# Performance work log

Measured on AMD Instinct MI355X. Metric: run time of the kernel, lower is better.

Reference implementation:

```python
import jax, jax.numpy as jnp
import numpy as np

D_MODEL = 1024
H = 16
D_K = D_MODEL // H
B = 4
S = 2048
NEG = -1.0e9


def setup_inputs() -> dict:
    key = jax.random.key(0)
    ks = jax.random.split(key, 12)
    scale = 1.0 / np.sqrt(D_MODEL)
    inp = {
        "q": jax.random.normal(ks[0], (B, S, D_MODEL), jnp.float32),
        "k": jax.random.normal(ks[1], (B, S, D_MODEL), jnp.float32),
        "v": jax.random.normal(ks[2], (B, S, D_MODEL), jnp.float32),
        "mask": jax.random.randint(ks[3], (1, 1, S, S), 0, 2, jnp.int32),
        # nn.Linear params: y = x @ W.T + b
        "Wq": jax.random.normal(ks[4], (D_MODEL, D_MODEL), jnp.float32) * scale,
        "bq": jnp.zeros((D_MODEL,), jnp.float32),
        "Wk": jax.random.normal(ks[5], (D_MODEL, D_MODEL), jnp.float32) * scale,
        "bk": jnp.zeros((D_MODEL,), jnp.float32),
        "Wv": jax.random.normal(ks[6], (D_MODEL, D_MODEL), jnp.float32) * scale,
        "bv": jnp.zeros((D_MODEL,), jnp.float32),
        "Wo": jax.random.normal(ks[7], (D_MODEL, D_MODEL), jnp.float32) * scale,
        "bo": jnp.zeros((D_MODEL,), jnp.float32),
    }
    return inp


def reference(q, k, v, mask, Wq, bq, Wk, bk, Wv, bv, Wo, bo):
    # QKV projections (torch Linear: x @ W.T + b)
    query = q @ Wq.T + bq                       # [B,S,D]
    key_ = k @ Wk.T + bk
    value = v @ Wv.T + bv
    # [B,S,D] -> [B,H,S,d_k]
    def split_heads(x):
        return x.reshape(B, S, H, D_K).transpose(0, 2, 1, 3)
    query, key_, value = split_heads(query), split_heads(key_), split_heads(value)
    # scaled dot-product attention
    scores = jnp.einsum("bhqd,bhkd->bhqk", query, key_) / np.sqrt(D_K)
    scores = jnp.where(mask == 0, NEG, scores)  # masked_fill(mask==0, -1e9)
    attn = jax.nn.softmax(scores, axis=-1)      # dropout p=0 -> identity
    x = jnp.einsum("bhqk,bhkd->bhqd", attn, value)
    # merge heads and output projection
    x = x.transpose(0, 2, 1, 3).reshape(B, S, D_MODEL)
    return x @ Wo.T + bo
```

## Files before the change

kernel.cpp:

```cpp
#include <hip/hip_runtime.h>
#include <hip/hip_bf16.h>

typedef __bf16 bf16;
typedef __bf16 bf16x8 __attribute__((ext_vector_type(8)));
typedef __bf16 bf16x4 __attribute__((ext_vector_type(4)));
typedef float  f32x4v __attribute__((ext_vector_type(4)));

#define MFMA16(a, b, c) __builtin_amdgcn_mfma_f32_16x16x32_bf16((a), (b), (c), 0, 0, 0)

static constexpr int D_MODEL = 1024;
static constexpr int NH      = 16;
static constexpr int DK      = 64;
static constexpr int BATCH   = 4;
static constexpr int SEQ     = 2048;

__device__ __forceinline__ void glds16(const void* g, void* l) {
    __builtin_amdgcn_global_load_lds((const __attribute__((address_space(1))) void*)g,
                                     (__attribute__((address_space(3))) void*)l, 16, 0, 0);
}

struct CvtArgs {
    const float* s[7];
    bf16* d[7];
    int n[7];
};

__global__ __launch_bounds__(256) void cvt7(CvtArgs a) {
    const int which = blockIdx.y;
    const int i = (blockIdx.x * 256 + threadIdx.x) * 8;
    if (i >= a.n[which]) return;
    const float4 v0 = *(const float4*)(a.s[which] + i);
    const float4 v1 = *(const float4*)(a.s[which] + i + 4);
    bf16x8 o = {(bf16)v0.x, (bf16)v0.y, (bf16)v0.z, (bf16)v0.w,
                (bf16)v1.x, (bf16)v1.y, (bf16)v1.z, (bf16)v1.w};
    *(bf16x8*)(a.d[which] + i) = o;
}

__global__ __launch_bounds__(256) void mask_prep(const int* __restrict__ m,
                                                 bf16* __restrict__ Mr) {
    const int o = blockIdx.x * 256 + threadIdx.x;
    const int row = o >> 11, j = o & 2047;
    const int g = j >> 6, idx = j & 63;
    const int incol = (g << 6) + ((idx & 3) << 4) + (idx >> 2);
    Mr[o] = m[row * 2048 + incol] ? (bf16)0.0f : (bf16)-16384.0f;
}

template <int MODE>
__global__ __launch_bounds__(256) void gemm_bt(const bf16* __restrict__ A,
                                               const bf16* __restrict__ W,
                                               const float* __restrict__ bias,
                                               void* __restrict__ outv) {
    __shared__ bf16 Als[128 * 32];
    __shared__ bf16 Bls[128 * 32];

    const int tid  = threadIdx.x;
    const int wave = tid >> 6;
    const int lane = tid & 63;
    const int l15  = lane & 15;
    const int quad = lane >> 4;
    const int m0   = blockIdx.y * 128;
    const int n0   = blockIdx.x * 128;
    const int wm   = (wave >> 1) * 64;
    const int wn   = (wave & 1) * 64;

    f32x4v acc[4][4];
#pragma unroll
    for (int i = 0; i < 4; ++i)
#pragma unroll
        for (int j = 0; j < 4; ++j) acc[i][j] = (f32x4v){0.f, 0.f, 0.f, 0.f};

    const int r_a    = wave * 16 + (lane >> 2);
    const int c_a    = (lane & 3) * 8;
    const int ldsoff = wave * 512;

    for (int k0 = 0; k0 < 1024; k0 += 32) {
        __syncthreads();
#pragma unroll
        for (int p = 0; p < 2; ++p) {
            const int row = p * 64 + r_a;
            glds16(A + (size_t)(m0 + row) * 1024 + k0 + c_a, &Als[p * 2048 + ldsoff]);
            glds16(W + (size_t)(n0 + row) * 1024 + k0 + c_a, &Bls[p * 2048 + ldsoff]);
        }
        __syncthreads();

        bf16x8 af[4], bfr[4];
#pragma unroll
        for (int i = 0; i < 4; ++i)
            af[i] = *(const bf16x8*)(&Als[(wm + i * 16 + l15) * 32 + quad * 8]);
#pragma unroll
        for (int j = 0; j < 4; ++j)
            bfr[j] = *(const bf16x8*)(&Bls[(wn + j * 16 + l15) * 32 + quad * 8]);
#pragma unroll
        for (int i = 0; i < 4; ++i)
#pragma unroll
            for (int j = 0; j < 4; ++j) acc[i][j] = MFMA16(af[i], bfr[j], acc[i][j]);
    }

#pragma unroll
    for (int j = 0; j < 4; ++j) {
        const int col = n0 + wn + j * 16 + l15;
        const float bs = bias[col];
        const int h = col >> 6, dk = col & 63;
        if (MODE == 1) {
            bf16* out = (bf16*)outv;
            const int sg = m0 + wm;
            const int bb = sg >> 11, sb = sg & 2047;
            const size_t rowbase = ((size_t)((bb * NH + h) * 64 + dk)) * SEQ + sb;
#pragma unroll
            for (int reg = 0; reg < 4; ++reg) {
                bf16x4 v = {(bf16)(acc[0][j][reg] + bs), (bf16)(acc[1][j][reg] + bs),
                            (bf16)(acc[2][j][reg] + bs), (bf16)(acc[3][j][reg] + bs)};
                *(bf16x4*)(&out[rowbase + (quad * 4 + reg) * 4]) = v;
            }
        } else {
#pragma unroll
            for (int i = 0; i < 4; ++i) {
                const int r4 = m0 + wm + i * 16 + quad * 4;
                const int b = r4 >> 11, sb = r4 & 2047;
                if (MODE == 2) {
                    float* out = (float*)outv;
#pragma unroll
                    for (int reg = 0; reg < 4; ++reg)
                        out[(size_t)(r4 + reg) * 1024 + col] = acc[i][j][reg] + bs;
                } else {
                    bf16* out = (bf16*)outv;
#pragma unroll
                    for (int reg = 0; reg < 4; ++reg)
                        out[((size_t)(b * NH + h) * SEQ + sb + reg) * 64 + dk] =
                            (bf16)(acc[i][j][reg] + bs);
                }
            }
        }
    }
}

__global__ __launch_bounds__(256, 4) void attn_kernel(const bf16* __restrict__ Qh,
                                                      const bf16* __restrict__ Kh,
                                                      const bf16* __restrict__ Vtg,
                                                      const bf16* __restrict__ Mr,
                                                      bf16* __restrict__ Xout) {
    __shared__ bf16 Kls[4096];
    __shared__ bf16 Vls[4096];
    __shared__ bf16 Pls[256 * 72];

    const int tid  = threadIdx.x;
    const int wave = tid >> 6;
    const int lane = tid & 63;
    const int l15  = lane & 15;
    const int quad = lane >> 4;
    const int bh   = blockIdx.x;
    const int q0   = blockIdx.y * 256;

    const size_t base = (size_t)bh * SEQ * DK;
    const bf16* Q  = Qh + base;
    const bf16* K  = Kh + base;
    const bf16* Vg = Vtg + base;

    const int qw = q0 + wave * 64;
    bf16x8 aq[4][2];
#pragma unroll
    for (int rb = 0; rb < 4; ++rb)
#pragma unroll
        for (int hf = 0; hf < 2; ++hf)
            aq[rb][hf] = *(const bf16x8*)(Q + (size_t)(qw + rb * 16 + l15) * 64 +
                                          hf * 32 + quad * 8);

    bf16x8 ones;
#pragma unroll
    for (int t = 0; t < 8; ++t) ones[t] = (bf16)1.0f;

    f32x4v acc[4][4];
    f32x4v sacc[4];
#pragma unroll
    for (int rb = 0; rb < 4; ++rb) {
        sacc[rb] = (f32x4v){0.f, 0.f, 0.f, 0.f};
#pragma unroll
        for (int x = 0; x < 4; ++x) acc[rb][x] = (f32x4v){0.f, 0.f, 0.f, 0.f};
    }

    constexpr float CLOG = 0.125f * 1.4426950408889634f;
    const bf16* mbase = Mr + (size_t)(qw + quad * 4) * 2048 + l15 * 4;

    for (int kt = 0; kt < SEQ; kt += 64) {
        __syncthreads();
#pragma unroll
        for (int p = 0; p < 2; ++p) {
            const int kc = wave * 2 + p;
            glds16(K + (size_t)(kt + lane) * 64 + kc * 8, &Kls[kc * 512]);
            glds16(Vg + (size_t)lane * SEQ + kt + kc * 8, &Vls[kc * 512]);
        }
        bf16x4 mv[4][4];
#pragma unroll
        for (int rb = 0; rb < 4; ++rb)
#pragma unroll
            for (int reg = 0; reg < 4; ++reg)
                mv[rb][reg] =
                    *(const bf16x4*)(mbase + (size_t)(rb * 16 + reg) * 2048 + kt);
        __syncthreads();

        bf16x8 bk[4][2];
#pragma unroll
        for (int n16 = 0; n16 < 4; ++n16)
#pragma unroll
            for (int kk = 0; kk < 2; ++kk)
                bk[n16][kk] = *(const bf16x8*)(&Kls[((kk * 4 + quad) * 64 + n16 * 16 + l15) * 8]);

#pragma unroll
        for (int rb = 0; rb < 4; ++rb) {
            f32x4v sv[4];
            __builtin_amdgcn_s_setprio(1);
#pragma unroll
            for (int n16 = 0; n16 < 4; ++n16) {
                f32x4v t = (f32x4v){0.f, 0.f, 0.f, 0.f};
                t = MFMA16(aq[rb][0], bk[n16][0], t);
                t = MFMA16(aq[rb][1], bk[n16][1], t);
                sv[n16] = t;
            }
            __builtin_amdgcn_s_setprio(0);
            const int prow0 = wave * 64 + rb * 16 + quad * 4;
#pragma unroll
            for (int reg = 0; reg < 4; ++reg) {
                const float e0 = exp2f(fmaf(sv[0][reg], CLOG, (float)mv[rb][reg][0]));
                const float e1 = exp2f(fmaf(sv[1][reg], CLOG, (float)mv[rb][reg][1]));
                const float e2 = exp2f(fmaf(sv[2][reg], CLOG, (float)mv[rb][reg][2]));
                const float e3 = exp2f(fmaf(sv[3][reg], CLOG, (float)mv[rb][reg][3]));
                bf16x4 p4 = {(bf16)e0, (bf16)e1, (bf16)e2, (bf16)e3};
                *(bf16x4*)(&Pls[(prow0 + reg) * 72 + l15 * 4]) = p4;
            }
        }

        bf16x8 pf[4][2];
#pragma unroll
        for (int rb = 0; rb < 4; ++rb)
#pragma unroll
            for (int kc2 = 0; kc2 < 2; ++kc2)
                pf[rb][kc2] = *(const bf16x8*)(&Pls[(wave * 64 + rb * 16 + l15) * 72 +
                                                    kc2 * 32 + quad * 8]);

        __builtin_amdgcn_s_setprio(1);
#pragma unroll
        for (int rb = 0; rb < 4; ++rb) {
            sacc[rb] = MFMA16(pf[rb][0], ones, sacc[rb]);
            sacc[rb] = MFMA16(pf[rb][1], ones, sacc[rb]);
        }
#pragma unroll
        for (int nt = 0; nt < 4; ++nt) {
            const bf16x8 bv0 = *(const bf16x8*)(&Vls[(quad * 64 + nt * 16 + l15) * 8]);
            const bf16x8 bv1 = *(const bf16x8*)(&Vls[((4 + quad) * 64 + nt * 16 + l15) * 8]);
#pragma unroll
            for (int rb = 0; rb < 4; ++rb) {
                acc[rb][nt] = MFMA16(pf[rb][0], bv0, acc[rb][nt]);
                acc[rb][nt] = MFMA16(pf[rb][1], bv1, acc[rb][nt]);
            }
        }
        __builtin_amdgcn_s_setprio(0);
    }

    const int b = bh >> 4, h = bh & 15;
#pragma unroll
    for (int rb = 0; rb < 4; ++rb) {
        float rinv[4];
#pragma unroll
        for (int reg = 0; reg < 4; ++reg) rinv[reg] = 1.0f / sacc[rb][reg];
#pragma unroll
        for (int nt = 0; nt < 4; ++nt)
#pragma unroll
            for (int reg = 0; reg < 4; ++reg) {
                const int sg = qw + rb * 16 + quad * 4 + reg;
                Xout[(size_t)(b * SEQ + sg) * D_MODEL + h * 64 + nt * 16 + l15] =
                    (bf16)(acc[rb][nt][reg] * rinv[reg]);
            }
    }
}

extern "C" void kernel_launch(void* const* d_in, const int* in_sizes, int n_in,
                              void* d_out, int out_size, void* d_ws, size_t ws_size,
                              hipStream_t stream) {
    const float* q    = (const float*)d_in[0];
    const float* k    = (const float*)d_in[1];
    const float* v    = (const float*)d_in[2];
    const int*   mask = (const int*)d_in[3];
    const float* Wq   = (const float*)d_in[4];
    const float* bq   = (const float*)d_in[5];
    const float* Wk   = (const float*)d_in[6];
    const float* bk   = (const float*)d_in[7];
    const float* Wv   = (const float*)d_in[8];
    const float* bv   = (const float*)d_in[9];
    const float* Wo   = (const float*)d_in[10];
    const float* bo   = (const float*)d_in[11];

    const size_t T = (size_t)BATCH * SEQ * D_MODEL;
    const size_t WN = (size_t)D_MODEL * D_MODEL;
    char* w = (char*)d_ws;
    bf16* Qh  = (bf16*)w;            w += T * 2;
    bf16* Kh  = (bf16*)w;            w += T * 2;
    bf16* Vt  = (bf16*)w;            w += T * 2;
    bf16* Mr  = (bf16*)w;            w += (size_t)SEQ * SEQ * 2;
    bf16* qb  = (bf16*)w;            w += T * 2;
    bf16* kb  = (bf16*)w;            w += T * 2;
    bf16* vb  = (bf16*)w;            w += T * 2;
    bf16* Wqb = (bf16*)w;            w += WN * 2;
    bf16* Wkb = (bf16*)w;            w += WN * 2;
    bf16* Wvb = (bf16*)w;            w += WN * 2;
    bf16* Wob = (bf16*)w;            w += WN * 2;

    CvtArgs ca;
    ca.s[0] = q;  ca.d[0] = qb;  ca.n[0] = (int)T;
    ca.s[1] = k;  ca.d[1] = kb;  ca.n[1] = (int)T;
    ca.s[2] = v;  ca.d[2] = vb;  ca.n[2] = (int)T;
    ca.s[3] = Wq; ca.d[3] = Wqb; ca.n[3] = (int)WN;
    ca.s[4] = Wk; ca.d[4] = Wkb; ca.n[4] = (int)WN;
    ca.s[5] = Wv; ca.d[5] = Wvb; ca.n[5] = (int)WN;
    ca.s[6] = Wo; ca.d[6] = Wob; ca.n[6] = (int)WN;

    cvt7<<<dim3(4096, 7), 256, 0, stream>>>(ca);
    mask_prep<<<dim3((SEQ * SEQ) / 256), 256, 0, stream>>>(mask, Mr);

    dim3 gg(D_MODEL / 128, (BATCH * SEQ) / 128);
    gemm_bt<0><<<gg, 256, 0, stream>>>(qb, Wqb, bq, (void*)Qh);
    gemm_bt<0><<<gg, 256, 0, stream>>>(kb, Wkb, bk, (void*)Kh);
    gemm_bt<1><<<gg, 256, 0, stream>>>(vb, Wvb, bv, (void*)Vt);

    attn_kernel<<<dim3(BATCH * NH, SEQ / 256), 256, 0, stream>>>(Qh, Kh, Vt, Mr, qb);

    gemm_bt<2><<<gg, 256, 0, stream>>>(qb, Wob, bo, d_out);
}
```

Baseline: 428.4 us.

## Keep softmax probabilities in registers by computing transposed scores, dropping LDS round-trip

The attention kernel now computes S^T by swapping MFMA operands (K as A, Q as B). Each lane's score outputs then line up with the A-operand layout needed for the P·V MFMA, so the Pls shared-memory staging buffer and its write/read round-trip are removed. The mask permutation, the V-transpose store pattern and the V LDS indexing are updated to match the new layout, and mask loads become wider 16-byte vectors. The GEMM launches switch to a 1D grid with a grouped block swizzle for L2 reuse, and attention launch bounds drop to 2 blocks per SIMD, which allows more registers but risks lower occupancy.

After: 391.7 us. 1.09x faster.

```diff
diff --git a/kernel.cpp b/kernel.cpp
--- a/kernel.cpp
+++ b/kernel.cpp
@@ -41,7 +41,7 @@
     const int o = blockIdx.x * 256 + threadIdx.x;
     const int row = o >> 11, j = o & 2047;
     const int g = j >> 6, idx = j & 63;
-    const int incol = (g << 6) + ((idx & 3) << 4) + (idx >> 2);
+    const int incol = (g << 6) + (((idx >> 2) & 3) << 4) + ((idx >> 4) << 2) + (idx & 3);
     Mr[o] = m[row * 2048 + incol] ? (bf16)0.0f : (bf16)-16384.0f;
 }
 
@@ -58,8 +58,9 @@
     const int lane = tid & 63;
     const int l15  = lane & 15;
     const int quad = lane >> 4;
-    const int m0   = blockIdx.y * 128;
-    const int n0   = blockIdx.x * 128;
+    const int L    = blockIdx.x;
+    const int m0   = ((L & 7) | ((L >> 6) << 3)) * 128;
+    const int n0   = ((L >> 3) & 7) * 128;
     const int wm   = (wave >> 1) * 64;
     const int wn   = (wave & 1) * 64;
 
@@ -107,10 +108,10 @@
             const int bb = sg >> 11, sb = sg & 2047;
             const size_t rowbase = ((size_t)((bb * NH + h) * 64 + dk)) * SEQ + sb;
 #pragma unroll
-            for (int reg = 0; reg < 4; ++reg) {
-                bf16x4 v = {(bf16)(acc[0][j][reg] + bs), (bf16)(acc[1][j][reg] + bs),
-                            (bf16)(acc[2][j][reg] + bs), (bf16)(acc[3][j][reg] + bs)};
-                *(bf16x4*)(&out[rowbase + (quad * 4 + reg) * 4]) = v;
+            for (int i = 0; i < 4; ++i) {
+                bf16x4 v = {(bf16)(acc[i][j][0] + bs), (bf16)(acc[i][j][1] + bs),
+                            (bf16)(acc[i][j][2] + bs), (bf16)(acc[i][j][3] + bs)};
+                *(bf16x4*)(&out[rowbase + quad * 16 + i * 4]) = v;
             }
         } else {
 #pragma unroll
@@ -134,14 +135,13 @@
     }
 }
 
-__global__ __launch_bounds__(256, 4) void attn_kernel(const bf16* __restrict__ Qh,
+__global__ __launch_bounds__(256, 2) void attn_kernel(const bf16* __restrict__ Qh,
                                                       const bf16* __restrict__ Kh,
                                                       const bf16* __restrict__ Vtg,
                                                       const bf16* __restrict__ Mr,
                                                       bf16* __restrict__ Xout) {
     __shared__ bf16 Kls[4096];
     __shared__ bf16 Vls[4096];
-    __shared__ bf16 Pls[256 * 72];
 
     const int tid  = threadIdx.x;
     const int wave = tid >> 6;
@@ -161,9 +161,9 @@
 #pragma unroll
     for (int rb = 0; rb < 4; ++rb)
 #pragma unroll
-        for (int hf = 0; hf < 2; ++hf)
-            aq[rb][hf] = *(const bf16x8*)(Q + (size_t)(qw + rb * 16 + l15) * 64 +
-                                          hf * 32 + quad * 8);
+        for (int kk = 0; kk < 2; ++kk)
+            aq[rb][kk] = *(const bf16x8*)(Q + (size_t)(qw + rb * 16 + l15) * 64 +
+                                          kk * 32 + quad * 8);
 
     bf16x8 ones;
 #pragma unroll
@@ -179,7 +179,7 @@
     }
 
     constexpr float CLOG = 0.125f * 1.4426950408889634f;
-    const bf16* mbase = Mr + (size_t)(qw + quad * 4) * 2048 + l15 * 4;
+    const bf16* mbase = Mr + (size_t)(qw + l15) * 2048 + quad * 16;
 
     for (int kt = 0; kt < SEQ; kt += 64) {
         __syncthreads();
@@ -189,22 +189,23 @@
             glds16(K + (size_t)(kt + lane) * 64 + kc * 8, &Kls[kc * 512]);
             glds16(Vg + (size_t)lane * SEQ + kt + kc * 8, &Vls[kc * 512]);
         }
-        bf16x4 mv[4][4];
+        bf16x8 mv[4][2];
 #pragma unroll
         for (int rb = 0; rb < 4; ++rb)
 #pragma unroll
-            for (int reg = 0; reg < 4; ++reg)
-                mv[rb][reg] =
-                    *(const bf16x4*)(mbase + (size_t)(rb * 16 + reg) * 2048 + kt);
+            for (int h2 = 0; h2 < 2; ++h2)
+                mv[rb][h2] = *(const bf16x8*)(mbase + (size_t)(rb * 16) * 2048 +
+                                              kt + h2 * 8);
         __syncthreads();
 
-        bf16x8 bk[4][2];
+        bf16x8 ak[4][2];
 #pragma unroll
         for (int n16 = 0; n16 < 4; ++n16)
 #pragma unroll
             for (int kk = 0; kk < 2; ++kk)
-                bk[n16][kk] = *(const bf16x8*)(&Kls[((kk * 4 + quad) * 64 + n16 * 16 + l15) * 8]);
-
+                ak[n16][kk] = *(const bf16x8*)(&Kls[((kk * 4 + quad) * 64 + n16 * 16 + l15) * 8]);
+
+        bf16x8 pa[4][2];
 #pragma unroll
         for (int rb = 0; rb < 4; ++rb) {
             f32x4v sv[4];
@@ -212,45 +213,35 @@
 #pragma unroll
             for (int n16 = 0; n16 < 4; ++n16) {
                 f32x4v t = (f32x4v){0.f, 0.f, 0.f, 0.f};
-                t = MFMA16(aq[rb][0], bk[n16][0], t);
-                t = MFMA16(aq[rb][1], bk[n16][1], t);
+                t = MFMA16(ak[n16][0], aq[rb][0], t);
+                t = MFMA16(ak[n16][1], aq[rb][1], t);
                 sv[n16] = t;
             }
             __builtin_amdgcn_s_setprio(0);
-            const int prow0 = wave * 64 + rb * 16 + quad * 4;
-#pragma unroll
-            for (int reg = 0; reg < 4; ++reg) {
-                const float e0 = exp2f(fmaf(sv[0][reg], CLOG, (float)mv[rb][reg][0]));
-                const float e1 = exp2f(fmaf(sv[1][reg], CLOG, (float)mv[rb][reg][1]));
-                const float e2 = exp2f(fmaf(sv[2][reg], CLOG, (float)mv[rb][reg][2]));
-                const float e3 = exp2f(fmaf(sv[3][reg], CLOG, (float)mv[rb][reg][3]));
-                bf16x4 p4 = {(bf16)e0, (bf16)e1, (bf16)e2, (bf16)e3};
-                *(bf16x4*)(&Pls[(prow0 + reg) * 72 + l15 * 4]) = p4;
-            }
-        }
-
-        bf16x8 pf[4][2];
-#pragma unroll
-        for (int rb = 0; rb < 4; ++rb)
-#pragma unroll
-            for (int kc2 = 0; kc2 < 2; ++kc2)
-                pf[rb][kc2] = *(const bf16x8*)(&Pls[(wave * 64 + rb * 16 + l15) * 72 +
-                                                    kc2 * 32 + quad * 8]);
+#pragma unroll
+            for (int n16 = 0; n16 < 4; ++n16)
+#pragma unroll
+                for (int reg = 0; reg < 4; ++reg) {
+                    const float e = exp2f(fmaf(sv[n16][reg], CLOG,
+                                               (float)mv[rb][n16 >> 1][(n16 & 1) * 4 + reg]));
+                    pa[rb][n16 >> 1][(n16 & 1) * 4 + reg] = (bf16)e;
+                }
+        }
 
         __builtin_amdgcn_s_setprio(1);
 #pragma unroll
         for (int rb = 0; rb < 4; ++rb) {
-            sacc[rb] = MFMA16(pf[rb][0], ones, sacc[rb]);
-            sacc[rb] = MFMA16(pf[rb][1], ones, sacc[rb]);
+            sacc[rb] = MFMA16(pa[rb][0], ones, sacc[rb]);
+            sacc[rb] = MFMA16(pa[rb][1], ones, sacc[rb]);
         }
 #pragma unroll
         for (int nt = 0; nt < 4; ++nt) {
-            const bf16x8 bv0 = *(const bf16x8*)(&Vls[(quad * 64 + nt * 16 + l15) * 8]);
-            const bf16x8 bv1 = *(const bf16x8*)(&Vls[((4 + quad) * 64 + nt * 16 + l15) * 8]);
+            const bf16x8 bv0 = *(const bf16x8*)(&Vls[((quad * 2 + 0) * 64 + nt * 16 + l15) * 8]);
+            const bf16x8 bv1 = *(const bf16x8*)(&Vls[((quad * 2 + 1) * 64 + nt * 16 + l15) * 8]);
 #pragma unroll
             for (int rb = 0; rb < 4; ++rb) {
-                acc[rb][nt] = MFMA16(pf[rb][0], bv0, acc[rb][nt]);
-                acc[rb][nt] = MFMA16(pf[rb][1], bv1, acc[rb][nt]);
+                acc[rb][nt] = MFMA16(pa[rb][0], bv0, acc[rb][nt]);
+                acc[rb][nt] = MFMA16(pa[rb][1], bv1, acc[rb][nt]);
             }
         }
         __builtin_amdgcn_s_setprio(0);
@@ -316,7 +307,7 @@
     cvt7<<<dim3(4096, 7), 256, 0, stream>>>(ca);
     mask_prep<<<dim3((SEQ * SEQ) / 256), 256, 0, stream>>>(mask, Mr);
 
-    dim3 gg(D_MODEL / 128, (BATCH * SEQ) / 128);
+    dim3 gg(512);
     gemm_bt<0><<<gg, 256, 0, stream>>>(qb, Wqb, bq, (void*)Qh);
     gemm_bt<0><<<gg, 256, 0, stream>>>(kb, Wkb, bk, (void*)Kh);
     gemm_bt<1><<<gg, 256, 0, stream>>>(vb, Wvb, bv, (void*)Vt);
```
